# Optimization experiments

Hardware: AMD Instinct MI355X
Metric: run time of the kernel (lower is better)

Reference implementation:

```python
import jax, jax.numpy as jnp
import numpy as np

HIDDEN = 2048
B, T, K = 64, 512, 49  # K = 7x7 spatial grid

def setup_inputs() -> dict:
    key = jax.random.key(0)
    ks = jax.random.split(key, 7)
    def xavier(k, shape):
        fan_in, fan_out = shape[1], shape[0]
        bound = float(np.sqrt(6.0 / (fan_in + fan_out)))
        return jax.random.uniform(k, shape, jnp.float32, -bound, bound)
    return {
        "V": jax.random.normal(ks[0], (B, K, HIDDEN), jnp.float32),
        "h_t": jax.random.normal(ks[1], (B, T, HIDDEN), jnp.float32),
        "sent_t": jax.random.normal(ks[2], (B, T, HIDDEN), jnp.float32),
        "Wv": xavier(ks[3], (K, HIDDEN)),
        "Wg": xavier(ks[4], (K, HIDDEN)),
        "Ws": xavier(ks[5], (K, HIDDEN)),
        "Wh": xavier(ks[6], (1, K)),
    }

def reference(V, h_t, sent_t, Wv, Wg, Ws, Wh):
    # Dropout is identity (eval mode / deterministic reference).
    wh = Wh[0]                                    # [K]
    pv = jnp.einsum('bkd,jd->bkj', V, Wv)         # [B,K,K]
    pg = jnp.einsum('btd,jd->btj', h_t, Wg)       # [B,T,K]
    content_v = pv[:, None, :, :] + pg[:, :, None, :]   # [B,T,K,K]
    z_t = jnp.tanh(content_v) @ wh                # [B,T,K]
    alpha_t = jax.nn.softmax(z_t, axis=-1)        # spatial attention
    c_t = jnp.einsum('btk,bkd->btd', alpha_t, V)  # [B,T,HIDDEN]
    content_s = jnp.einsum('btd,jd->btj', sent_t, Ws) + pg  # [B,T,K]
    z_ext = jnp.tanh(content_s) @ wh              # [B,T]
    extend = jnp.concatenate([z_t, z_ext[..., None]], axis=-1)  # [B,T,K+1]
    alpha_hat = jax.nn.softmax(extend, axis=-1)
    beta_t = alpha_hat[:, :, -1:]                 # sentinel gate [B,T,1]
    c_hat_t = beta_t * sent_t + (1.0 - beta_t) * c_t
    return (c_hat_t, alpha_t, beta_t)
```

## Files before the change

### kernel.cpp

```cpp
#include <hip/hip_runtime.h>

#define HIDDEN 2048
#define NB 64
#define NT 512
#define NK 49

typedef __attribute__((ext_vector_type(4))) float f32x4;
typedef __attribute__((ext_vector_type(8))) short short8;

__device__ __forceinline__ unsigned cvtpk_bf16(float a, float b) {
    unsigned r;
    asm("v_cvt_pk_bf16_f32 %0, %1, %2" : "=v"(r) : "v"(a), "v"(b));
    return r;
}

__device__ __forceinline__ unsigned short f2bf(float x) {
    union { float f; unsigned u; } v; v.f = x;
    unsigned r = v.u + 0x7FFF + ((v.u >> 16) & 1);
    return (unsigned short)(r >> 16);
}

__global__ __launch_bounds__(256) void convert_w(
    const float* __restrict__ Wg, const float* __restrict__ Ws,
    const float* __restrict__ Wv, unsigned short* __restrict__ Wf)
{
    int tau = blockIdx.x * 256 + threadIdx.x;
    int m   = tau >> 14;
    int rem = tau & 16383;
    int c   = rem >> 12;
    int s   = (rem >> 6) & 63;
    int l   = rem & 63;
    int col = c * 16 + (l & 15);
    int k0  = s * 32 + ((l >> 4) << 3);

    const float* W = (m == 0) ? Wg : (m == 1) ? Ws : Wv;
    unsigned short out[8];
    if (col < NK) {
        const float* p = W + (size_t)col * HIDDEN + k0;
        #pragma unroll
        for (int j = 0; j < 8; j++) out[j] = f2bf(p[j]);
    } else {
        #pragma unroll
        for (int j = 0; j < 8; j++) out[j] = 0;
    }
    unsigned short* dst = Wf + (size_t)tau * 8;
    #pragma unroll
    for (int j = 0; j < 8; j++) dst[j] = out[j];
}

__global__ __launch_bounds__(256) void gemm_mfma(
    const float* __restrict__ h, const float* __restrict__ s,
    const float* __restrict__ V, const unsigned short* __restrict__ Wf,
    float* __restrict__ pg, float* __restrict__ ps, float* __restrict__ pv)
{
    int w = threadIdx.x >> 6, lane = threadIdx.x & 63;
    int gw = blockIdx.x * 4 + w;

    const float* A; float* C; int rowBase; const unsigned short* wf;
    if (gw < 2048)      { A = h; C = pg; rowBase = gw * 16;          wf = Wf; }
    else if (gw < 4096) { A = s; C = ps; rowBase = (gw - 2048) * 16; wf = Wf + (size_t)16384 * 8; }
    else                { A = V; C = pv; rowBase = (gw - 4096) * 16; wf = Wf + (size_t)32768 * 8; }

    const float* ap = A + (size_t)(rowBase + (lane & 15)) * HIDDEN + ((lane >> 4) << 3);
    const short8* bp = (const short8*)(wf + (size_t)lane * 8);

    f32x4 acc0 = {0.f, 0.f, 0.f, 0.f};
    f32x4 acc1 = acc0, acc2 = acc0, acc3 = acc0;

    #pragma unroll 2
    for (int st = 0; st < 64; st++) {
        float4 f0 = *(const float4*)(ap + st * 32);
        float4 f1 = *(const float4*)(ap + st * 32 + 4);

        union { short8 v; unsigned u[4]; } a;
        a.u[0] = cvtpk_bf16(f0.x, f0.y);
        a.u[1] = cvtpk_bf16(f0.z, f0.w);
        a.u[2] = cvtpk_bf16(f1.x, f1.y);
        a.u[3] = cvtpk_bf16(f1.z, f1.w);

        short8 b0 = bp[(0 * 64 + st) * 64];
        short8 b1 = bp[(1 * 64 + st) * 64];
        short8 b2 = bp[(2 * 64 + st) * 64];
        short8 b3 = bp[(3 * 64 + st) * 64];

        acc0 = __builtin_amdgcn_mfma_f32_16x16x32_bf16(a.v, b0, acc0, 0, 0, 0);
        acc1 = __builtin_amdgcn_mfma_f32_16x16x32_bf16(a.v, b1, acc1, 0, 0, 0);
        acc2 = __builtin_amdgcn_mfma_f32_16x16x32_bf16(a.v, b2, acc2, 0, 0, 0);
        acc3 = __builtin_amdgcn_mfma_f32_16x16x32_bf16(a.v, b3, acc3, 0, 0, 0);
    }

    int colb  = lane & 15;
    int rquad = (lane >> 4) << 2;
    float* crow = C + (size_t)(rowBase + rquad) * NK + colb;
    #pragma unroll
    for (int r = 0; r < 4; r++) {
        crow[(size_t)r * NK + 0]  = acc0[r];
        crow[(size_t)r * NK + 16] = acc1[r];
        crow[(size_t)r * NK + 32] = acc2[r];
    }
    if (colb == 0) {
        #pragma unroll
        for (int r = 0; r < 4; r++) crow[(size_t)r * NK + 48] = acc3[r];
    }
}

__device__ __forceinline__ float ftanh(float x) {
    float e = __expf(2.f * x);
    return 1.f - 2.f * __builtin_amdgcn_rcpf(e + 1.f);
}

__global__ __launch_bounds__(256) void zab_kernel(
    const float* __restrict__ pg, const float* __restrict__ ps,
    const float* __restrict__ pv, const float* __restrict__ Wh,
    float* __restrict__ alpha, float* __restrict__ beta)
{
    int w = threadIdx.x >> 6, lane = threadIdx.x & 63;
    int row = blockIdx.x * 4 + w;
    int b = row >> 9;

    const float* pgrow = pg + (size_t)row * NK;
    const float* psrow = ps + (size_t)row * NK;

    float va = 0.f;
    if (lane < NK)
        va = ftanh(psrow[lane] + pgrow[lane]) * Wh[lane];
    float z_ext = va;
    #pragma unroll
    for (int off = 32; off; off >>= 1) z_ext += __shfl_xor(z_ext, off);

    float z = -1e30f;
    if (lane < NK) {
        const float* pvrow = pv + ((size_t)b * NK + lane) * NK;
        float acc = 0.f;
        for (int j = 0; j < NK; j++)
            acc = fmaf(ftanh(pvrow[j] + pgrow[j]), Wh[j], acc);
        z = acc;
    }

    float m = z;
    #pragma unroll
    for (int off = 32; off; off >>= 1) m = fmaxf(m, __shfl_xor(m, off));
    float p = (lane < NK) ? __expf(z - m) : 0.f;
    float ssum = p;
    #pragma unroll
    for (int off = 32; off; off >>= 1) ssum += __shfl_xor(ssum, off);
    float a = p * __builtin_amdgcn_rcpf(ssum);

    if (lane < NK)
        alpha[(size_t)row * NK + lane] = a;

    float me = fmaxf(m, z_ext);
    float se = ssum * __expf(m - me) + __expf(z_ext - me);
    float bet = __expf(z_ext - me) * __builtin_amdgcn_rcpf(se);
    if (lane == 0) beta[row] = bet;
}

__global__ __launch_bounds__(256) void chat_kernel(
    const float* __restrict__ V, const float* __restrict__ sent,
    const float* __restrict__ alpha, const float* __restrict__ beta,
    float* __restrict__ chat)
{
    int d0 = blockIdx.x * 128;
    int t0 = blockIdx.y * 32;
    int b  = blockIdx.z;

    __shared__ float alpha_s[NK][36];
    __shared__ float beta_s[32];

    int tid = threadIdx.x;

    const float* arow = alpha + ((size_t)b * NT + t0) * NK;
    for (int i = tid; i < 32 * NK; i += 256) {
        int t = i / NK, k = i - t * NK;
        alpha_s[k][t] = arow[i];
    }
    if (tid < 32) beta_s[tid] = beta[(size_t)b * NT + t0 + tid];
    __syncthreads();

    int tx = tid & 31;
    int ty = tid >> 5;

    const float* vp = V + (size_t)b * NK * HIDDEN + d0 + tx * 4;

    float4 acc[4];
    #pragma unroll
    for (int i = 0; i < 4; i++) acc[i] = make_float4(0.f, 0.f, 0.f, 0.f);

    #pragma unroll 7
    for (int k = 0; k < NK; k++) {
        float4 vv = *(const float4*)(vp + (size_t)k * HIDDEN);
        float4 a4 = *(const float4*)&alpha_s[k][ty * 4];
        acc[0].x = fmaf(a4.x, vv.x, acc[0].x);
        acc[0].y = fmaf(a4.x, vv.y, acc[0].y);
        acc[0].z = fmaf(a4.x, vv.z, acc[0].z);
        acc[0].w = fmaf(a4.x, vv.w, acc[0].w);
        acc[1].x = fmaf(a4.y, vv.x, acc[1].x);
        acc[1].y = fmaf(a4.y, vv.y, acc[1].y);
        acc[1].z = fmaf(a4.y, vv.z, acc[1].z);
        acc[1].w = fmaf(a4.y, vv.w, acc[1].w);
        acc[2].x = fmaf(a4.z, vv.x, acc[2].x);
        acc[2].y = fmaf(a4.z, vv.y, acc[2].y);
        acc[2].z = fmaf(a4.z, vv.z, acc[2].z);
        acc[2].w = fmaf(a4.z, vv.w, acc[2].w);
        acc[3].x = fmaf(a4.w, vv.x, acc[3].x);
        acc[3].y = fmaf(a4.w, vv.y, acc[3].y);
        acc[3].z = fmaf(a4.w, vv.z, acc[3].z);
        acc[3].w = fmaf(a4.w, vv.w, acc[3].w);
    }

    #pragma unroll
    for (int i = 0; i < 4; i++) {
        int t = ty * 4 + i;
        float bt = beta_s[t];
        const float* sp = sent + ((size_t)b * NT + t0 + t) * HIDDEN + d0 + tx * 4;
        float*       op = chat + ((size_t)b * NT + t0 + t) * HIDDEN + d0 + tx * 4;
        float4 sv = *(const float4*)sp;
        float4 o;
        o.x = fmaf(bt, sv.x, (1.f - bt) * acc[i].x);
        o.y = fmaf(bt, sv.y, (1.f - bt) * acc[i].y);
        o.z = fmaf(bt, sv.z, (1.f - bt) * acc[i].z);
        o.w = fmaf(bt, sv.w, (1.f - bt) * acc[i].w);
        *(float4*)op = o;
    }
}

extern "C" void kernel_launch(void* const* d_in, const int* in_sizes, int n_in,
                              void* d_out, int out_size, void* d_ws, size_t ws_size,
                              hipStream_t stream)
{
    const float* V    = (const float*)d_in[0];
    const float* h_t  = (const float*)d_in[1];
    const float* sent = (const float*)d_in[2];
    const float* Wv   = (const float*)d_in[3];
    const float* Wg   = (const float*)d_in[4];
    const float* Ws   = (const float*)d_in[5];
    const float* Wh   = (const float*)d_in[6];

    float* out   = (float*)d_out;
    float* chat  = out;
    float* alpha = out + (size_t)NB * NT * HIDDEN;
    float* beta  = alpha + (size_t)NB * NT * NK;

    float* ws = (float*)d_ws;
    float* pg = ws;
    float* ps = pg + (size_t)NB * NT * NK;
    float* pv = ps + (size_t)NB * NT * NK;
    unsigned short* Wf = (unsigned short*)(pv + (size_t)NB * NK * NK);

    convert_w<<<192, 256, 0, stream>>>(Wg, Ws, Wv, Wf);
    gemm_mfma<<<1073, 256, 0, stream>>>(h_t, sent, V, Wf, pg, ps, pv);
    zab_kernel<<<(NB * NT) / 4, 256, 0, stream>>>(pg, ps, pv, Wh, alpha, beta);
    chat_kernel<<<dim3(HIDDEN / 128, NT / 32, NB), 256, 0, stream>>>(V, sent, alpha, beta, chat);
}
```

Before: 387.0 us.

## Tile projection GEMM through LDS with double-buffered A/B and async B loads

The per-wave streaming MFMA GEMM becomes a block-tiled GEMM. Each block covers 128 rows, converts A to bf16 into swizzled, double-buffered LDS, and pulls the pre-packed B weights into LDS with global_load_lds, prefetching the next chunk while computing. The weight packing order changes to match. zab_kernel also stages the per-batch pv matrix transposed in LDS, so the 49-wide inner loop reads coalesced shared memory instead of strided global loads. The aim is to cut redundant B global traffic and improve latency hiding, at the cost of more LDS use and barriers per chunk.

```diff
diff --git a/kernel.cpp b/kernel.cpp
--- a/kernel.cpp
+++ b/kernel.cpp
@@ -5,6 +5,10 @@
 #define NT 512
 #define NK 49
 
+#define BM 128
+#define BK 64
+#define NCH (HIDDEN/BK)
+
 typedef __attribute__((ext_vector_type(4))) float f32x4;
 typedef __attribute__((ext_vector_type(8))) short short8;
 
@@ -27,11 +31,11 @@
     int tau = blockIdx.x * 256 + threadIdx.x;
     int m   = tau >> 14;
     int rem = tau & 16383;
-    int c   = rem >> 12;
-    int s   = (rem >> 6) & 63;
+    int st  = rem >> 8;
+    int c   = (rem >> 6) & 3;
     int l   = rem & 63;
     int col = c * 16 + (l & 15);
-    int k0  = s * 32 + ((l >> 4) << 3);
+    int k0  = st * 32 + ((l >> 4) << 3);
 
     const float* W = (m == 0) ? Wg : (m == 1) ? Ws : Wv;
     unsigned short out[8];
@@ -53,54 +57,128 @@
     const float* __restrict__ V, const unsigned short* __restrict__ Wf,
     float* __restrict__ pg, float* __restrict__ ps, float* __restrict__ pv)
 {
-    int w = threadIdx.x >> 6, lane = threadIdx.x & 63;
-    int gw = blockIdx.x * 4 + w;
-
-    const float* A; float* C; int rowBase; const unsigned short* wf;
-    if (gw < 2048)      { A = h; C = pg; rowBase = gw * 16;          wf = Wf; }
-    else if (gw < 4096) { A = s; C = ps; rowBase = (gw - 2048) * 16; wf = Wf + (size_t)16384 * 8; }
-    else                { A = V; C = pv; rowBase = (gw - 4096) * 16; wf = Wf + (size_t)32768 * 8; }
-
-    const float* ap = A + (size_t)(rowBase + (lane & 15)) * HIDDEN + ((lane >> 4) << 3);
-    const short8* bp = (const short8*)(wf + (size_t)lane * 8);
-
-    f32x4 acc0 = {0.f, 0.f, 0.f, 0.f};
-    f32x4 acc1 = acc0, acc2 = acc0, acc3 = acc0;
-
-    #pragma unroll 2
-    for (int st = 0; st < 64; st++) {
-        float4 f0 = *(const float4*)(ap + st * 32);
-        float4 f1 = *(const float4*)(ap + st * 32 + 4);
-
-        union { short8 v; unsigned u[4]; } a;
-        a.u[0] = cvtpk_bf16(f0.x, f0.y);
-        a.u[1] = cvtpk_bf16(f0.z, f0.w);
-        a.u[2] = cvtpk_bf16(f1.x, f1.y);
-        a.u[3] = cvtpk_bf16(f1.z, f1.w);
-
-        short8 b0 = bp[(0 * 64 + st) * 64];
-        short8 b1 = bp[(1 * 64 + st) * 64];
-        short8 b2 = bp[(2 * 64 + st) * 64];
-        short8 b3 = bp[(3 * 64 + st) * 64];
-
-        acc0 = __builtin_amdgcn_mfma_f32_16x16x32_bf16(a.v, b0, acc0, 0, 0, 0);
-        acc1 = __builtin_amdgcn_mfma_f32_16x16x32_bf16(a.v, b1, acc1, 0, 0, 0);
-        acc2 = __builtin_amdgcn_mfma_f32_16x16x32_bf16(a.v, b2, acc2, 0, 0, 0);
-        acc3 = __builtin_amdgcn_mfma_f32_16x16x32_bf16(a.v, b3, acc3, 0, 0, 0);
-    }
+    int tid = threadIdx.x;
+    int w = tid >> 6, lane = tid & 63;
+    int blk = blockIdx.x;
+
+    const float* A; float* C; int rowBase; const unsigned short* wfm; int Mrows;
+    if (blk < 256)      { A = h; C = pg; rowBase = blk * BM;         wfm = Wf;                     Mrows = 32768; }
+    else if (blk < 512) { A = s; C = ps; rowBase = (blk - 256) * BM; wfm = Wf + (size_t)16384 * 8; Mrows = 32768; }
+    else                { A = V; C = pv; rowBase = (blk - 512) * BM; wfm = Wf + (size_t)32768 * 8; Mrows = 3136;  }
+
+    __shared__ unsigned short Abf[2][BM * BK];
+    __shared__ short8        Bb[2][8 * 64];
+
+    const short8* wfp = (const short8*)wfm;
+
+    int ar    = tid >> 1;
+    int ahalf = tid & 1;
+    int agr   = rowBase + ar; if (agr > Mrows - 1) agr = Mrows - 1;
+    const float* aprow = A + (size_t)agr * HIDDEN + ahalf * 32;
+
+    f32x4 acc00 = {0.f,0.f,0.f,0.f}, acc01 = acc00, acc02 = acc00, acc03 = acc00;
+    f32x4 acc10 = acc00, acc11 = acc00, acc12 = acc00, acc13 = acc00;
+
+    float4 g0, g1, g2, g3, g4, g5, g6, g7;
+
+#define ALOAD(ch) { \
+    const float4* _p = (const float4*)(aprow + (size_t)(ch) * BK); \
+    g0 = _p[0]; g1 = _p[1]; g2 = _p[2]; g3 = _p[3]; \
+    g4 = _p[4]; g5 = _p[5]; g6 = _p[6]; g7 = _p[7]; }
+
+#define AWRITE(buf) { \
+    char* _base = (char*)&Abf[buf][0] + ar * 128; \
+    int _rk = (ar & 7) << 4; \
+    uint2 v; \
+    v.x = cvtpk_bf16(g0.x, g0.y); v.y = cvtpk_bf16(g0.z, g0.w); \
+    *(uint2*)(_base + ((ahalf*64 + 0)  ^ _rk)) = v; \
+    v.x = cvtpk_bf16(g1.x, g1.y); v.y = cvtpk_bf16(g1.z, g1.w); \
+    *(uint2*)(_base + ((ahalf*64 + 8)  ^ _rk)) = v; \
+    v.x = cvtpk_bf16(g2.x, g2.y); v.y = cvtpk_bf16(g2.z, g2.w); \
+    *(uint2*)(_base + ((ahalf*64 + 16) ^ _rk)) = v; \
+    v.x = cvtpk_bf16(g3.x, g3.y); v.y = cvtpk_bf16(g3.z, g3.w); \
+    *(uint2*)(_base + ((ahalf*64 + 24) ^ _rk)) = v; \
+    v.x = cvtpk_bf16(g4.x, g4.y); v.y = cvtpk_bf16(g4.z, g4.w); \
+    *(uint2*)(_base + ((ahalf*64 + 32) ^ _rk)) = v; \
+    v.x = cvtpk_bf16(g5.x, g5.y); v.y = cvtpk_bf16(g5.z, g5.w); \
+    *(uint2*)(_base + ((ahalf*64 + 40) ^ _rk)) = v; \
+    v.x = cvtpk_bf16(g6.x, g6.y); v.y = cvtpk_bf16(g6.z, g6.w); \
+    *(uint2*)(_base + ((ahalf*64 + 48) ^ _rk)) = v; \
+    v.x = cvtpk_bf16(g7.x, g7.y); v.y = cvtpk_bf16(g7.z, g7.w); \
+    *(uint2*)(_base + ((ahalf*64 + 56) ^ _rk)) = v; }
+
+#define BDMA(ch, buf) { \
+    const short8* _s0 = wfp + (size_t)(((ch) * 2 + 0) * 4 + w) * 64 + lane; \
+    const short8* _s1 = wfp + (size_t)(((ch) * 2 + 1) * 4 + w) * 64 + lane; \
+    __builtin_amdgcn_global_load_lds((const void*)_s0, (void*)&Bb[buf][(w)     * 64], 16, 0, 0); \
+    __builtin_amdgcn_global_load_lds((const void*)_s1, (void*)&Bb[buf][(w + 4) * 64], 16, 0, 0); }
+
+#define COMPUTE(buf) { \
+    const char*  _ab = (const char*)&Abf[buf][0]; \
+    const short8* _bb = &Bb[buf][0]; \
+    _Pragma("unroll") \
+    for (int st = 0; st < 2; st++) { \
+        int bir = st * 64 + ((lane >> 4) << 4); \
+        int r0 = w * 32 + (lane & 15); \
+        int r1 = r0 + 16; \
+        short8 a0 = *(const short8*)(_ab + r0 * 128 + (bir ^ ((r0 & 7) << 4))); \
+        short8 a1 = *(const short8*)(_ab + r1 * 128 + (bir ^ ((r1 & 7) << 4))); \
+        short8 b0 = _bb[(st * 4 + 0) * 64 + lane]; \
+        short8 b1 = _bb[(st * 4 + 1) * 64 + lane]; \
+        short8 b2 = _bb[(st * 4 + 2) * 64 + lane]; \
+        short8 b3 = _bb[(st * 4 + 3) * 64 + lane]; \
+        acc00 = __builtin_amdgcn_mfma_f32_16x16x32_bf16(a0, b0, acc00, 0, 0, 0); \
+        acc01 = __builtin_amdgcn_mfma_f32_16x16x32_bf16(a0, b1, acc01, 0, 0, 0); \
+        acc02 = __builtin_amdgcn_mfma_f32_16x16x32_bf16(a0, b2, acc02, 0, 0, 0); \
+        acc03 = __builtin_amdgcn_mfma_f32_16x16x32_bf16(a0, b3, acc03, 0, 0, 0); \
+        acc10 = __builtin_amdgcn_mfma_f32_16x16x32_bf16(a1, b0, acc10, 0, 0, 0); \
+        acc11 = __builtin_amdgcn_mfma_f32_16x16x32_bf16(a1, b1, acc11, 0, 0, 0); \
+        acc12 = __builtin_amdgcn_mfma_f32_16x16x32_bf16(a1, b2, acc12, 0, 0, 0); \
+        acc13 = __builtin_amdgcn_mfma_f32_16x16x32_bf16(a1, b3, acc13, 0, 0, 0); \
+    } }
+
+    ALOAD(0)
+    AWRITE(0)
+    BDMA(0, 0)
+    ALOAD(1)
+    __syncthreads();
+
+    #pragma unroll 1
+    for (int ch = 0; ch < NCH; ch++) {
+        int p = ch & 1;
+        if (ch + 1 < NCH) {
+            AWRITE(p ^ 1)
+            BDMA(ch + 1, p ^ 1)
+        }
+        if (ch + 2 < NCH) { ALOAD(ch + 2) }
+        COMPUTE(p)
+        __syncthreads();
+    }
+
+#undef ALOAD
+#undef AWRITE
+#undef BDMA
+#undef COMPUTE
 
     int colb  = lane & 15;
     int rquad = (lane >> 4) << 2;
-    float* crow = C + (size_t)(rowBase + rquad) * NK + colb;
-    #pragma unroll
-    for (int r = 0; r < 4; r++) {
-        crow[(size_t)r * NK + 0]  = acc0[r];
-        crow[(size_t)r * NK + 16] = acc1[r];
-        crow[(size_t)r * NK + 32] = acc2[r];
-    }
-    if (colb == 0) {
+    #pragma unroll
+    for (int m = 0; m < 2; m++) {
+        int rowb = rowBase + w * 32 + m * 16 + rquad;
+        float* crow = C + (size_t)rowb * NK + colb;
+        f32x4 a0 = m ? acc10 : acc00;
+        f32x4 a1 = m ? acc11 : acc01;
+        f32x4 a2 = m ? acc12 : acc02;
+        f32x4 a3 = m ? acc13 : acc03;
         #pragma unroll
-        for (int r = 0; r < 4; r++) crow[(size_t)r * NK + 48] = acc3[r];
+        for (int r = 0; r < 4; r++) {
+            if (rowb + r < Mrows) {
+                crow[(size_t)r * NK + 0]  = a0[r];
+                crow[(size_t)r * NK + 16] = a1[r];
+                crow[(size_t)r * NK + 32] = a2[r];
+                if (colb == 0) crow[(size_t)r * NK + 48] = a3[r];
+            }
+        }
     }
 }
 
@@ -118,6 +196,16 @@
     int row = blockIdx.x * 4 + w;
     int b = row >> 9;
 
+    __shared__ float pvT[NK * 52];
+    {
+        const float* pvb = pv + (size_t)b * NK * NK;
+        for (int i = threadIdx.x; i < NK * NK; i += 256) {
+            int k = i / NK, j = i - k * NK;
+            pvT[j * 52 + k] = pvb[i];
+        }
+    }
+    __syncthreads();
+
     const float* pgrow = pg + (size_t)row * NK;
     const float* psrow = ps + (size_t)row * NK;
 
@@ -130,10 +218,9 @@
 
     float z = -1e30f;
     if (lane < NK) {
-        const float* pvrow = pv + ((size_t)b * NK + lane) * NK;
         float acc = 0.f;
         for (int j = 0; j < NK; j++)
-            acc = fmaf(ftanh(pvrow[j] + pgrow[j]), Wh[j], acc);
+            acc = fmaf(ftanh(pvT[j * 52 + lane] + pgrow[j]), Wh[j], acc);
         z = acc;
     }
 
@@ -248,7 +335,7 @@
     unsigned short* Wf = (unsigned short*)(pv + (size_t)NB * NK * NK);
 
     convert_w<<<192, 256, 0, stream>>>(Wg, Ws, Wv, Wf);
-    gemm_mfma<<<1073, 256, 0, stream>>>(h_t, sent, V, Wf, pg, ps, pv);
+    gemm_mfma<<<537, 256, 0, stream>>>(h_t, sent, V, Wf, pg, ps, pv);
     zab_kernel<<<(NB * NT) / 4, 256, 0, stream>>>(pg, ps, pv, Wh, alpha, beta);
     chat_kernel<<<dim3(HIDDEN / 128, NT / 32, NB), 256, 0, stream>>>(V, sent, alpha, beta, chat);
 }
```

After: 393.1 us. Within noise of the previous version (+1.6%).

## Split-K the projection GEMM with atomic accumulation and stage pv transposed in LDS

Applied to the files above, without the earlier changes.

The projection GEMM now splits the 2048-long reduction into four chunks, one per wave, and quadruples the grid. Partial sums are combined with atomicAdd into a workspace that is zeroed by an added memset. The packed weight layout is reordered so that the four column tiles for each k-step sit next to each other. The zab kernel now loads the per-batch pv matrix transposed into shared memory so the inner loop reads are not strided. The split is meant to add parallelism to a memory-bound GEMM, at the cost of atomics, a memset and nondeterministic summation order.

```diff
diff --git a/kernel.cpp b/kernel.cpp
--- a/kernel.cpp
+++ b/kernel.cpp
@@ -27,11 +27,11 @@
     int tau = blockIdx.x * 256 + threadIdx.x;
     int m   = tau >> 14;
     int rem = tau & 16383;
-    int c   = rem >> 12;
-    int s   = (rem >> 6) & 63;
+    int st  = rem >> 8;
+    int c   = (rem >> 6) & 3;
     int l   = rem & 63;
     int col = c * 16 + (l & 15);
-    int k0  = s * 32 + ((l >> 4) << 3);
+    int k0  = st * 32 + ((l >> 4) << 3);
 
     const float* W = (m == 0) ? Wg : (m == 1) ? Ws : Wv;
     unsigned short out[8];
@@ -56,21 +56,27 @@
     int w = threadIdx.x >> 6, lane = threadIdx.x & 63;
     int gw = blockIdx.x * 4 + w;
 
-    const float* A; float* C; int rowBase; const unsigned short* wf;
-    if (gw < 2048)      { A = h; C = pg; rowBase = gw * 16;          wf = Wf; }
-    else if (gw < 4096) { A = s; C = ps; rowBase = (gw - 2048) * 16; wf = Wf + (size_t)16384 * 8; }
-    else                { A = V; C = pv; rowBase = (gw - 4096) * 16; wf = Wf + (size_t)32768 * 8; }
-
-    const float* ap = A + (size_t)(rowBase + (lane & 15)) * HIDDEN + ((lane >> 4) << 3);
-    const short8* bp = (const short8*)(wf + (size_t)lane * 8);
+    const float* A; float* C; int q; const unsigned short* wfm;
+    if (gw < 8192)       { A = h; C = pg; q = gw;         wfm = Wf; }
+    else if (gw < 16384) { A = s; C = ps; q = gw - 8192;  wfm = Wf + (size_t)16384 * 8; }
+    else                 { A = V; C = pv; q = gw - 16384; wfm = Wf + (size_t)32768 * 8; }
+
+    int rowBase = (q >> 2) * 16;
+    int split   = q & 3;
+
+    const float* ap = A + (size_t)(rowBase + (lane & 15)) * HIDDEN
+                        + ((lane >> 4) << 3) + split * 512;
+    const short8* bp = (const short8*)wfm + lane;
 
     f32x4 acc0 = {0.f, 0.f, 0.f, 0.f};
     f32x4 acc1 = acc0, acc2 = acc0, acc3 = acc0;
 
+    int st0 = split * 16;
+
     #pragma unroll 2
-    for (int st = 0; st < 64; st++) {
-        float4 f0 = *(const float4*)(ap + st * 32);
-        float4 f1 = *(const float4*)(ap + st * 32 + 4);
+    for (int i = 0; i < 16; i++) {
+        float4 f0 = *(const float4*)(ap + i * 32);
+        float4 f1 = *(const float4*)(ap + i * 32 + 4);
 
         union { short8 v; unsigned u[4]; } a;
         a.u[0] = cvtpk_bf16(f0.x, f0.y);
@@ -78,10 +84,11 @@
         a.u[2] = cvtpk_bf16(f1.x, f1.y);
         a.u[3] = cvtpk_bf16(f1.z, f1.w);
 
-        short8 b0 = bp[(0 * 64 + st) * 64];
-        short8 b1 = bp[(1 * 64 + st) * 64];
-        short8 b2 = bp[(2 * 64 + st) * 64];
-        short8 b3 = bp[(3 * 64 + st) * 64];
+        int st = st0 + i;
+        short8 b0 = bp[(size_t)(st * 4 + 0) * 64];
+        short8 b1 = bp[(size_t)(st * 4 + 1) * 64];
+        short8 b2 = bp[(size_t)(st * 4 + 2) * 64];
+        short8 b3 = bp[(size_t)(st * 4 + 3) * 64];
 
         acc0 = __builtin_amdgcn_mfma_f32_16x16x32_bf16(a.v, b0, acc0, 0, 0, 0);
         acc1 = __builtin_amdgcn_mfma_f32_16x16x32_bf16(a.v, b1, acc1, 0, 0, 0);
@@ -94,13 +101,14 @@
     float* crow = C + (size_t)(rowBase + rquad) * NK + colb;
     #pragma unroll
     for (int r = 0; r < 4; r++) {
-        crow[(size_t)r * NK + 0]  = acc0[r];
-        crow[(size_t)r * NK + 16] = acc1[r];
-        crow[(size_t)r * NK + 32] = acc2[r];
+        atomicAdd(&crow[(size_t)r * NK + 0],  acc0[r]);
+        atomicAdd(&crow[(size_t)r * NK + 16], acc1[r]);
+        atomicAdd(&crow[(size_t)r * NK + 32], acc2[r]);
     }
     if (colb == 0) {
         #pragma unroll
-        for (int r = 0; r < 4; r++) crow[(size_t)r * NK + 48] = acc3[r];
+        for (int r = 0; r < 4; r++)
+            atomicAdd(&crow[(size_t)r * NK + 48], acc3[r]);
     }
 }
 
@@ -118,6 +126,16 @@
     int row = blockIdx.x * 4 + w;
     int b = row >> 9;
 
+    __shared__ float pvT[NK * 52];
+    {
+        const float* pvb = pv + (size_t)b * NK * NK;
+        for (int i = threadIdx.x; i < NK * NK; i += 256) {
+            int k = i / NK, j = i - k * NK;
+            pvT[j * 52 + k] = pvb[i];
+        }
+    }
+    __syncthreads();
+
     const float* pgrow = pg + (size_t)row * NK;
     const float* psrow = ps + (size_t)row * NK;
 
@@ -130,10 +148,9 @@
 
     float z = -1e30f;
     if (lane < NK) {
-        const float* pvrow = pv + ((size_t)b * NK + lane) * NK;
         float acc = 0.f;
         for (int j = 0; j < NK; j++)
-            acc = fmaf(ftanh(pvrow[j] + pgrow[j]), Wh[j], acc);
+            acc = fmaf(ftanh(pvT[j * 52 + lane] + pgrow[j]), Wh[j], acc);
         z = acc;
     }
 
@@ -247,8 +264,11 @@
     float* pv = ps + (size_t)NB * NT * NK;
     unsigned short* Wf = (unsigned short*)(pv + (size_t)NB * NK * NK);
 
+    size_t accBytes = ((size_t)NB * NT * NK * 2 + (size_t)NB * NK * NK) * sizeof(float);
+    hipMemsetAsync((void*)pg, 0, accBytes, stream);
+
     convert_w<<<192, 256, 0, stream>>>(Wg, Ws, Wv, Wf);
-    gemm_mfma<<<1073, 256, 0, stream>>>(h_t, sent, V, Wf, pg, ps, pv);
+    gemm_mfma<<<4292, 256, 0, stream>>>(h_t, sent, V, Wf, pg, ps, pv);
     zab_kernel<<<(NB * NT) / 4, 256, 0, stream>>>(pg, ps, pv, Wh, alpha, beta);
     chat_kernel<<<dim3(HIDDEN / 128, NT / 32, NB), 256, 0, stream>>>(V, sent, alpha, beta, chat);
 }
```

After: 400.0 us. 3.4% more time.

## Stage bf16 weight fragments in LDS for GEMM and transpose pv in zab

Applied to the files above, without the earlier changes.

The GEMM no longer has every wave read its bf16 weight fragments straight from global memory. Each block now loads a 64KB chunk of weights into LDS with global_load_lds, four chunks in total with barriers between them, and the waves read B from LDS. The convert_w layout is reordered so each chunk is contiguous. In zab_kernel, each block transposes the batch's 49x49 pv tile into padded shared memory, so lane reads are conflict-free and coalesced instead of strided global loads. The cost is 64KB of LDS per block, which caps occupancy, plus barriers that stall MFMA work while chunks load.

```diff
diff --git a/kernel.cpp b/kernel.cpp
--- a/kernel.cpp
+++ b/kernel.cpp
@@ -27,11 +27,11 @@
     int tau = blockIdx.x * 256 + threadIdx.x;
     int m   = tau >> 14;
     int rem = tau & 16383;
-    int c   = rem >> 12;
-    int s   = (rem >> 6) & 63;
+    int st  = rem >> 8;
+    int c   = (rem >> 6) & 3;
     int l   = rem & 63;
     int col = c * 16 + (l & 15);
-    int k0  = s * 32 + ((l >> 4) << 3);
+    int k0  = st * 32 + ((l >> 4) << 3);
 
     const float* W = (m == 0) ? Wg : (m == 1) ? Ws : Wv;
     unsigned short out[8];
@@ -56,37 +56,53 @@
     int w = threadIdx.x >> 6, lane = threadIdx.x & 63;
     int gw = blockIdx.x * 4 + w;
 
-    const float* A; float* C; int rowBase; const unsigned short* wf;
-    if (gw < 2048)      { A = h; C = pg; rowBase = gw * 16;          wf = Wf; }
-    else if (gw < 4096) { A = s; C = ps; rowBase = (gw - 2048) * 16; wf = Wf + (size_t)16384 * 8; }
-    else                { A = V; C = pv; rowBase = (gw - 4096) * 16; wf = Wf + (size_t)32768 * 8; }
+    const float* A; float* C; int rowBase; const unsigned short* wfm;
+    if (gw < 2048)      { A = h; C = pg; rowBase = gw * 16;          wfm = Wf; }
+    else if (gw < 4096) { A = s; C = ps; rowBase = (gw - 2048) * 16; wfm = Wf + (size_t)16384 * 8; }
+    else                { A = V; C = pv; rowBase = (gw - 4096) * 16; wfm = Wf + (size_t)32768 * 8; }
 
     const float* ap = A + (size_t)(rowBase + (lane & 15)) * HIDDEN + ((lane >> 4) << 3);
-    const short8* bp = (const short8*)(wf + (size_t)lane * 8);
+    const short8* wfp = (const short8*)wfm;
+
+    __shared__ short8 Bs[64 * 64];
 
     f32x4 acc0 = {0.f, 0.f, 0.f, 0.f};
     f32x4 acc1 = acc0, acc2 = acc0, acc3 = acc0;
 
-    #pragma unroll 2
-    for (int st = 0; st < 64; st++) {
-        float4 f0 = *(const float4*)(ap + st * 32);
-        float4 f1 = *(const float4*)(ap + st * 32 + 4);
-
-        union { short8 v; unsigned u[4]; } a;
-        a.u[0] = cvtpk_bf16(f0.x, f0.y);
-        a.u[1] = cvtpk_bf16(f0.z, f0.w);
-        a.u[2] = cvtpk_bf16(f1.x, f1.y);
-        a.u[3] = cvtpk_bf16(f1.z, f1.w);
-
-        short8 b0 = bp[(0 * 64 + st) * 64];
-        short8 b1 = bp[(1 * 64 + st) * 64];
-        short8 b2 = bp[(2 * 64 + st) * 64];
-        short8 b3 = bp[(3 * 64 + st) * 64];
-
-        acc0 = __builtin_amdgcn_mfma_f32_16x16x32_bf16(a.v, b0, acc0, 0, 0, 0);
-        acc1 = __builtin_amdgcn_mfma_f32_16x16x32_bf16(a.v, b1, acc1, 0, 0, 0);
-        acc2 = __builtin_amdgcn_mfma_f32_16x16x32_bf16(a.v, b2, acc2, 0, 0, 0);
-        acc3 = __builtin_amdgcn_mfma_f32_16x16x32_bf16(a.v, b3, acc3, 0, 0, 0);
+    #pragma unroll 1
+    for (int S = 0; S < 4; S++) {
+        __syncthreads();
+        #pragma unroll
+        for (int i = 0; i < 16; i++) {
+            int f = w * 16 + i;
+            __builtin_amdgcn_global_load_lds(
+                (const void*)(wfp + (size_t)(S * 64 + f) * 64 + lane),
+                (void*)&Bs[f * 64], 16, 0, 0);
+        }
+        __syncthreads();
+
+        #pragma unroll 2
+        for (int t = 0; t < 16; t++) {
+            int st = S * 16 + t;
+            float4 f0 = *(const float4*)(ap + st * 32);
+            float4 f1 = *(const float4*)(ap + st * 32 + 4);
+
+            union { short8 v; unsigned u[4]; } a;
+            a.u[0] = cvtpk_bf16(f0.x, f0.y);
+            a.u[1] = cvtpk_bf16(f0.z, f0.w);
+            a.u[2] = cvtpk_bf16(f1.x, f1.y);
+            a.u[3] = cvtpk_bf16(f1.z, f1.w);
+
+            short8 b0 = Bs[(t * 4 + 0) * 64 + lane];
+            short8 b1 = Bs[(t * 4 + 1) * 64 + lane];
+            short8 b2 = Bs[(t * 4 + 2) * 64 + lane];
+            short8 b3 = Bs[(t * 4 + 3) * 64 + lane];
+
+            acc0 = __builtin_amdgcn_mfma_f32_16x16x32_bf16(a.v, b0, acc0, 0, 0, 0);
+            acc1 = __builtin_amdgcn_mfma_f32_16x16x32_bf16(a.v, b1, acc1, 0, 0, 0);
+            acc2 = __builtin_amdgcn_mfma_f32_16x16x32_bf16(a.v, b2, acc2, 0, 0, 0);
+            acc3 = __builtin_amdgcn_mfma_f32_16x16x32_bf16(a.v, b3, acc3, 0, 0, 0);
+        }
     }
 
     int colb  = lane & 15;
@@ -118,6 +134,16 @@
     int row = blockIdx.x * 4 + w;
     int b = row >> 9;
 
+    __shared__ float pvT[NK * 52];
+    {
+        const float* pvb = pv + (size_t)b * NK * NK;
+        for (int i = threadIdx.x; i < NK * NK; i += 256) {
+            int k = i / NK, j = i - k * NK;
+            pvT[j * 52 + k] = pvb[i];
+        }
+    }
+    __syncthreads();
+
     const float* pgrow = pg + (size_t)row * NK;
     const float* psrow = ps + (size_t)row * NK;
 
@@ -130,10 +156,9 @@
 
     float z = -1e30f;
     if (lane < NK) {
-        const float* pvrow = pv + ((size_t)b * NK + lane) * NK;
         float acc = 0.f;
         for (int j = 0; j < NK; j++)
-            acc = fmaf(ftanh(pvrow[j] + pgrow[j]), Wh[j], acc);
+            acc = fmaf(ftanh(pvT[j * 52 + lane] + pgrow[j]), Wh[j], acc);
         z = acc;
     }
 
```

After: 394.8 us. 1.02x slower.
